# Kernel tuning notes

Measured on AMD Instinct MI355X. Metric: run time of the kernel, lower is better.

## Reference

```python
import jax, jax.numpy as jnp
import numpy as np

# Static config matching init_kwargs
DG = 8          # deformable groups
KH, KW = 3, 3
STRIDE, PAD, DIL = 1, 1, 1


def setup_inputs() -> dict:
    key = jax.random.key(0)
    k1, k2, k3, k4 = jax.random.split(key, 4)
    B, C, H, W = 4, 128, 128, 128
    Cout = 128
    K = KH * KW
    x = jax.random.normal(k1, (B, C, H, W), dtype=jnp.float32)
    offset = jax.random.normal(k2, (B, 2 * DG * K, H, W), dtype=jnp.float32)
    mask = jax.random.uniform(k3, (B, DG * K, H, W), dtype=jnp.float32)
    stdv = 1.0 / np.sqrt(C * KH * KW)
    weight = jax.random.uniform(k4, (Cout, C, KH, KW), dtype=jnp.float32,
                                minval=-stdv, maxval=stdv)
    bias = jnp.zeros((Cout,), dtype=jnp.float32)
    return {"x": x, "offset": offset, "mask": mask, "weight": weight, "bias": bias}


def _deform_conv2d(x, offset, mask, weight, bias):
    B, C, H, W = x.shape
    Cout = weight.shape[0]
    K = KH * KW
    Ho = (H + 2 * PAD - DIL * (KH - 1) - 1) // STRIDE + 1
    Wo = (W + 2 * PAD - DIL * (KW - 1) - 1) // STRIDE + 1
    Cg = C // DG

    # offsets: channel layout [dg, k, (dy, dx)]
    off = offset.reshape(B, DG, K, 2, Ho, Wo)
    dy, dx = off[:, :, :, 0], off[:, :, :, 1]          # [B, DG, K, Ho, Wo]
    m = mask.reshape(B, DG, K, Ho, Wo)

    ky, kx = jnp.meshgrid(jnp.arange(KH), jnp.arange(KW), indexing='ij')
    ky, kx = ky.reshape(K), kx.reshape(K)
    # base sampling grid per kernel tap: [K, Ho] / [K, Wo]
    py = (jnp.arange(Ho) * STRIDE - PAD)[None, :] + (ky * DIL)[:, None]
    px = (jnp.arange(Wo) * STRIDE - PAD)[None, :] + (kx * DIL)[:, None]

    sy = dy + py[None, None, :, :, None].astype(dy.dtype)  # [B, DG, K, Ho, Wo]
    sx = dx + px[None, None, :, None, :].astype(dx.dtype)

    y0f = jnp.floor(sy); x0f = jnp.floor(sx)
    ly = sy - y0f; lx = sx - x0f
    y0 = y0f.astype(jnp.int32); x0 = x0f.astype(jnp.int32)

    x_g = x.reshape(B, DG, Cg, H * W)

    def gather(iy, ix):
        valid = ((iy >= 0) & (iy < H) & (ix >= 0) & (ix < W)).astype(x.dtype)
        idx = jnp.clip(iy, 0, H - 1) * W + jnp.clip(ix, 0, W - 1)
        flat = idx.reshape(B, DG, 1, K * Ho * Wo)
        v = jnp.take_along_axis(x_g, flat, axis=3).reshape(B, DG, Cg, K, Ho, Wo)
        return v * valid[:, :, None]

    w00 = ((1 - ly) * (1 - lx))[:, :, None]
    w01 = ((1 - ly) * lx)[:, :, None]
    w10 = (ly * (1 - lx))[:, :, None]
    w11 = (ly * lx)[:, :, None]

    val = (gather(y0, x0) * w00 + gather(y0, x0 + 1) * w01 +
           gather(y0 + 1, x0) * w10 + gather(y0 + 1, x0 + 1) * w11)
    val = val * m[:, :, None]                         # modulation
    sampled = val.reshape(B, C, K, Ho, Wo)

    w = weight.reshape(Cout, C, K)
    out = jnp.einsum('bckhw,ock->bohw', sampled, w)
    return out + bias[None, :, None, None]


def reference(x, offset, mask, weight, bias):
    return _deform_conv2d(x, offset, mask, weight, bias)
```

## Files before the change

### kernel.cpp

```cpp
#include <hip/hip_runtime.h>
#include <hip/hip_fp16.h>


#define NB    4
#define NC    128
#define NH    128
#define NW    128
#define NCOUT 128
#define NDG   8
#define NCG   16
#define NK    9
#define NCK   1152
#define NHW   16384
#define GK    160
#define ROWP  168

typedef __attribute__((ext_vector_type(4))) float f32x4;
typedef _Float16 half8 __attribute__((ext_vector_type(8)));

union C16 { uint4 u[2]; __half2 h[8]; };

__device__ __forceinline__ unsigned pk2h(float a, float b) {
  return (unsigned)__half_as_ushort(__float2half_rn(a)) |
         ((unsigned)__half_as_ushort(__float2half_rn(b)) << 16);
}

__global__ __launch_bounds__(256)
void prep(const float* __restrict__ x, const float* __restrict__ w,
          ushort* __restrict__ xt, ushort* __restrict__ wf) {
  __shared__ __align__(16) unsigned LDSU[1024 * 9];
  const int tid = threadIdx.x;

  if (blockIdx.x < 128) {
    const int o = blockIdx.x;
    float* WL = (float*)LDSU;
    const float4* src = (const float4*)(w + o * NCK);
    for (int i = tid; i < NCK / 4; i += 256) ((float4*)WL)[i] = src[i];
    __syncthreads();
    unsigned* dstw = (unsigned*)wf;
    for (int t = tid; t < 640; t += 256) {
      const int g = t / 80, r = t - g * 80;
      unsigned v = 0;
      if (r < 72) {
        const int k = r >> 3;
        const int c = g * NCG + (r & 7) * 2;
        v = pk2h(WL[c * NK + k], WL[(c + 1) * NK + k]);
      }
      const int ks = r >> 4;
      const int kq = (r >> 2) & 3;
      const int ep = r & 3;
      dstw[((((g * 5 + ks) * 4 + kq) * 128) + o) * 4 + ep] = v;
    }
  } else {
    const int blk  = blockIdx.x - 128;
    const int slab = blk >> 4;
    const int hw0  = (blk & 15) * 1024;
    const float* xb = x + (size_t)slab * NCG * NHW + hw0;
#pragma unroll
    for (int cp = 0; cp < 8; ++cp) {
#pragma unroll
      for (int i = 0; i < 4; ++i) {
        const int hw = tid + 256 * i;
        LDSU[hw * 9 + cp] =
            pk2h(xb[(2 * cp) * NHW + hw], xb[(2 * cp + 1) * NHW + hw]);
      }
    }
    __syncthreads();
    uint4* dst = (uint4*)(xt + ((size_t)slab * NHW + hw0) * NCG);
#pragma unroll
    for (int j = 0; j < 8; ++j) {
      const int lin = tid + 256 * j;
      const int hw = lin >> 1, q = lin & 1;
      uint4 v;
      v.x = LDSU[hw * 9 + q * 4 + 0];
      v.y = LDSU[hw * 9 + q * 4 + 1];
      v.z = LDSU[hw * 9 + q * 4 + 2];
      v.w = LDSU[hw * 9 + q * 4 + 3];
      dst[lin] = v;
    }
  }
}

__device__ __forceinline__ void sample_one(
    int p, int k, int g, int b, int ho, float dy, float dx, float mm,
    const ushort* __restrict__ xt, ushort* __restrict__ S) {
  const int ky = k / 3, kx = k - ky * 3;

  const float sy = dy + (float)(ho - 1 + ky);
  const float sx = dx + (float)(p - 1 + kx);
  const float y0f = floorf(sy), x0f = floorf(sx);
  const float ly = sy - y0f, lx = sx - x0f;
  const int y0 = (int)y0f, x0 = (int)x0f;
  const int y1 = y0 + 1,  x1 = x0 + 1;
  const float hy = 1.f - ly, hx = 1.f - lx;

  float w00 = hy * hx * mm, w01 = hy * lx * mm;
  float w10 = ly * hx * mm, w11 = ly * lx * mm;
  if (y0 < 0 || y0 >= NH) { w00 = 0.f; w01 = 0.f; }
  if (y1 < 0 || y1 >= NH) { w10 = 0.f; w11 = 0.f; }
  if (x0 < 0 || x0 >= NW) { w00 = 0.f; w10 = 0.f; }
  if (x1 < 0 || x1 >= NW) { w01 = 0.f; w11 = 0.f; }

  const int yc0 = min(max(y0, 0), NH - 1);
  const int yc1 = min(max(y1, 0), NH - 1);
  const int xc0 = min(max(x0, 0), NW - 1);
  const int xc1 = min(max(x1, 0), NW - 1);

  const ushort* xg = xt + (size_t)(b * NDG + g) * NHW * NCG;
  const uint4* q00 = (const uint4*)(xg + (yc0 * NW + xc0) * NCG);
  const uint4* q01 = (const uint4*)(xg + (yc0 * NW + xc1) * NCG);
  const uint4* q10 = (const uint4*)(xg + (yc1 * NW + xc0) * NCG);
  const uint4* q11 = (const uint4*)(xg + (yc1 * NW + xc1) * NCG);

  C16 v00, v01, v10, v11, r;
  v00.u[0] = q00[0]; v00.u[1] = q00[1];
  v01.u[0] = q01[0]; v01.u[1] = q01[1];
  v10.u[0] = q10[0]; v10.u[1] = q10[1];
  v11.u[0] = q11[0]; v11.u[1] = q11[1];

  const __half2 W00 = __float2half2_rn(w00);
  const __half2 W01 = __float2half2_rn(w01);
  const __half2 W10 = __float2half2_rn(w10);
  const __half2 W11 = __float2half2_rn(w11);
#pragma unroll
  for (int i = 0; i < 8; ++i) {
    __half2 a = __hmul2(v00.h[i], W00);
    a = __hfma2(v01.h[i], W01, a);
    a = __hfma2(v10.h[i], W10, a);
    a = __hfma2(v11.h[i], W11, a);
    r.h[i] = a;
  }
  ushort* dp = &S[p * ROWP + k * 16];
  *(uint4*)dp = r.u[0];
  *((uint4*)dp + 1) = r.u[1];
}

__global__ __launch_bounds__(512, 4)
void dcn_main(const float* __restrict__ off,
              const float* __restrict__ msk,
              const ushort* __restrict__ xt,
              const ushort* __restrict__ wf,
              const float* __restrict__ bias,
              float* __restrict__ out) {
  __shared__ __align__(16) ushort S[128 * ROWP];

  const int tid  = threadIdx.x;
  const int blk0 = blockIdx.x;
  const int blk  = (blk0 & 7) * 64 + (blk0 >> 3);
  const int b    = blk >> 7;
  const int ho   = blk & 127;

  const int lane = tid & 63;
  const int wv   = tid >> 6;
  const int l15  = lane & 15;
  const int kq   = lane >> 4;
  const int mh   = (wv & 1) * 4;
  const int nb   = wv >> 1;
  const int cbase = nb * 32 + l15;

  const float* offB = off + (size_t)b * 144 * NHW + ho * NW;
  const float* mskB = msk + (size_t)b * 72  * NHW + ho * NW;

  for (int i = tid; i < 128 * 8; i += 512) {
    ((unsigned*)S)[(i >> 3) * (ROWP / 2) + 72 + (i & 7)] = 0;
  }

  f32x4 acc[4][2];
#pragma unroll
  for (int m = 0; m < 4; ++m) {
    acc[m][0] = {0.f, 0.f, 0.f, 0.f};
    acc[m][1] = {0.f, 0.f, 0.f, 0.f};
  }

  const int p0 = tid & 127;
  const int k0 = tid >> 7;
  const int k1 = k0 + 4;

  float dy0, dx0, mm0, dy1, dx1, mm1, dy2 = 0.f, dx2 = 0.f, mm2 = 0.f;
  {
    dy0 = offB[(k0 * 2) * NHW + p0];
    dx0 = offB[(k0 * 2 + 1) * NHW + p0];
    mm0 = mskB[k0 * NHW + p0];
    dy1 = offB[(k1 * 2) * NHW + p0];
    dx1 = offB[(k1 * 2 + 1) * NHW + p0];
    mm1 = mskB[k1 * NHW + p0];
    if (tid < 128) {
      dy2 = offB[16 * NHW + p0];
      dx2 = offB[17 * NHW + p0];
      mm2 = mskB[8 * NHW + p0];
    }
  }

  for (int g = 0; g < 8; ++g) {
    if (g) __syncthreads();

    half8 bf0[5], bf1[5];
    {
      const ushort* wb = wf + ((size_t)(g * 20 + kq) * 128 + cbase) * 8;
#pragma unroll
      for (int ks = 0; ks < 5; ++ks) {
        bf0[ks] = *(const half8*)(wb + ks * 4096);
        bf1[ks] = *(const half8*)(wb + ks * 4096 + 128);
      }
    }

    sample_one(p0, k0, g, b, ho, dy0, dx0, mm0, xt, S);
    sample_one(p0, k1, g, b, ho, dy1, dx1, mm1, xt, S);
    if (tid < 128) sample_one(p0, 8, g, b, ho, dy2, dx2, mm2, xt, S);

    if (g < 7) {
      const int gka = (g + 1) * 9 + k0, gkb = (g + 1) * 9 + k1;
      dy0 = offB[(gka * 2) * NHW + p0];
      dx0 = offB[(gka * 2 + 1) * NHW + p0];
      mm0 = mskB[gka * NHW + p0];
      dy1 = offB[(gkb * 2) * NHW + p0];
      dx1 = offB[(gkb * 2 + 1) * NHW + p0];
      mm1 = mskB[gkb * NHW + p0];
      if (tid < 128) {
        const int gkc = (g + 1) * 9 + 8;
        dy2 = offB[(gkc * 2) * NHW + p0];
        dx2 = offB[(gkc * 2 + 1) * NHW + p0];
        mm2 = mskB[gkc * NHW + p0];
      }
    }
    __syncthreads();

    const ushort* sa = &S[l15 * ROWP + kq * 8];
#pragma unroll
    for (int ks = 0; ks < 5; ++ks) {
#pragma unroll
      for (int m = 0; m < 4; ++m) {
        const half8 a = *(const half8*)(sa + (mh + m) * 16 * ROWP + ks * 32);
        acc[m][0] = __builtin_amdgcn_mfma_f32_16x16x32_f16(a, bf0[ks], acc[m][0], 0, 0, 0);
        acc[m][1] = __builtin_amdgcn_mfma_f32_16x16x32_f16(a, bf1[ks], acc[m][1], 0, 0, 0);
      }
    }
  }

#pragma unroll
  for (int j = 0; j < 2; ++j) {
    const int c0 = nb * 32 + j * 16 + l15;
    const float bs = bias[c0];
    float* op = out + (size_t)(b * NCOUT + c0) * NHW + ho * NW + kq * 4;
#pragma unroll
    for (int m = 0; m < 4; ++m) {
      float4 r = {acc[m][j][0] + bs, acc[m][j][1] + bs,
                  acc[m][j][2] + bs, acc[m][j][3] + bs};
      *(float4*)(op + (mh + m) * 16) = r;
    }
  }
}

extern "C" void kernel_launch(void* const* d_in, const int* in_sizes, int n_in,
                              void* d_out, int out_size, void* d_ws, size_t ws_size,
                              hipStream_t stream) {
  const float* x    = (const float*)d_in[0];
  const float* off  = (const float*)d_in[1];
  const float* msk  = (const float*)d_in[2];
  const float* wgt  = (const float*)d_in[3];
  const float* bias = (const float*)d_in[4];
  float* out = (float*)d_out;

  ushort* xt = (ushort*)d_ws;
  ushort* wf = xt + (size_t)NB * NDG * NHW * NCG;

  hipLaunchKernelGGL(prep, dim3(640), dim3(256), 0, stream, x, wgt, xt, wf);
  hipLaunchKernelGGL(dcn_main, dim3(512), dim3(512), 0, stream,
                     off, msk, xt, wf, bias, out);
}
```

Baseline: 221.4 us.

## Switch GEMM stage to 32x32x16 MFMA with repacked weight fragments

Replaces the 16x16x32 MFMA tiling (4x2 tiles per wave, weights preloaded to registers) with 32x32x16 MFMA, two accumulators per wave. Weight fragments are repacked in prep into a layout matched to the new instruction and loaded per k-step inside the loop instead of being held in registers. The intent is fewer MFMA issues and LDS reads per FLOP and lower register pressure. In exchange, the weight global loads now sit on the critical path after the barrier, and the K dimension is padded to 160.

```diff
diff --git a/kernel.cpp b/kernel.cpp
--- a/kernel.cpp
+++ b/kernel.cpp
@@ -15,7 +15,7 @@
 #define GK    160
 #define ROWP  168
 
-typedef __attribute__((ext_vector_type(4))) float f32x4;
+typedef __attribute__((ext_vector_type(16))) float f32x16;
 typedef _Float16 half8 __attribute__((ext_vector_type(8)));
 
 union C16 { uint4 u[2]; __half2 h[8]; };
@@ -39,17 +39,18 @@
     __syncthreads();
     unsigned* dstw = (unsigned*)wf;
     for (int t = tid; t < 640; t += 256) {
-      const int g = t / 80, r = t - g * 80;
+      const int frag  = t >> 2;
+      const int pairI = t & 3;
+      const int khalf = frag & 1;
+      const int fk    = frag >> 1;
+      const int g     = fk / 10;
+      const int ks    = fk - g * 10;
       unsigned v = 0;
-      if (r < 72) {
-        const int k = r >> 3;
-        const int c = g * NCG + (r & 7) * 2;
-        v = pk2h(WL[c * NK + k], WL[(c + 1) * NK + k]);
+      if (ks < 9) {
+        const int c = g * NCG + khalf * 8 + pairI * 2;
+        v = pk2h(WL[c * NK + ks], WL[(c + 1) * NK + ks]);
       }
-      const int ks = r >> 4;
-      const int kq = (r >> 2) & 3;
-      const int ep = r & 3;
-      dstw[((((g * 5 + ks) * 4 + kq) * 128) + o) * 4 + ep] = v;
+      dstw[frag * 512 + o * 4 + pairI] = v;
     }
   } else {
     const int blk  = blockIdx.x - 128;
@@ -150,27 +151,23 @@
   const int b    = blk >> 7;
   const int ho   = blk & 127;
 
-  const int lane = tid & 63;
-  const int wv   = tid >> 6;
-  const int l15  = lane & 15;
-  const int kq   = lane >> 4;
-  const int mh   = (wv & 1) * 4;
-  const int nb   = wv >> 1;
-  const int cbase = nb * 32 + l15;
+  const int lane  = tid & 63;
+  const int wv    = tid >> 6;
+  const int l31   = lane & 31;
+  const int hi    = lane >> 5;
+  const int nbase = (wv & 3) * 32;
+  const int mpair = wv >> 2;
 
   const float* offB = off + (size_t)b * 144 * NHW + ho * NW;
   const float* mskB = msk + (size_t)b * 72  * NHW + ho * NW;
 
-  for (int i = tid; i < 128 * 8; i += 512) {
+  for (int i = tid; i < 1024; i += 512) {
     ((unsigned*)S)[(i >> 3) * (ROWP / 2) + 72 + (i & 7)] = 0;
   }
 
-  f32x4 acc[4][2];
-#pragma unroll
-  for (int m = 0; m < 4; ++m) {
-    acc[m][0] = {0.f, 0.f, 0.f, 0.f};
-    acc[m][1] = {0.f, 0.f, 0.f, 0.f};
-  }
+  f32x16 acc0, acc1;
+#pragma unroll
+  for (int i = 0; i < 16; ++i) { acc0[i] = 0.f; acc1[i] = 0.f; }
 
   const int p0 = tid & 127;
   const int k0 = tid >> 7;
@@ -193,16 +190,6 @@
 
   for (int g = 0; g < 8; ++g) {
     if (g) __syncthreads();
-
-    half8 bf0[5], bf1[5];
-    {
-      const ushort* wb = wf + ((size_t)(g * 20 + kq) * 128 + cbase) * 8;
-#pragma unroll
-      for (int ks = 0; ks < 5; ++ks) {
-        bf0[ks] = *(const half8*)(wb + ks * 4096);
-        bf1[ks] = *(const half8*)(wb + ks * 4096 + 128);
-      }
-    }
 
     sample_one(p0, k0, g, b, ho, dy0, dx0, mm0, xt, S);
     sample_one(p0, k1, g, b, ho, dy1, dx1, mm1, xt, S);
@@ -225,28 +212,32 @@
     }
     __syncthreads();
 
-    const ushort* sa = &S[l15 * ROWP + kq * 8];
-#pragma unroll
-    for (int ks = 0; ks < 5; ++ks) {
-#pragma unroll
-      for (int m = 0; m < 4; ++m) {
-        const half8 a = *(const half8*)(sa + (mh + m) * 16 * ROWP + ks * 32);
-        acc[m][0] = __builtin_amdgcn_mfma_f32_16x16x32_f16(a, bf0[ks], acc[m][0], 0, 0, 0);
-        acc[m][1] = __builtin_amdgcn_mfma_f32_16x16x32_f16(a, bf1[ks], acc[m][1], 0, 0, 0);
-      }
-    }
-  }
-
+    const ushort* wb  = wf + ((size_t)(g * 10) * 2 + hi) * 1024
+                           + (nbase + l31) * 8;
+    const ushort* sa0 = &S[(mpair * 64 + l31) * ROWP + hi * 8];
+    const ushort* sa1 = sa0 + 32 * ROWP;
+#pragma unroll
+    for (int ks = 0; ks < 10; ++ks) {
+      const half8 bfrag = *(const half8*)(wb + ks * 2048);
+      const half8 a0 = *(const half8*)(sa0 + ks * 16);
+      const half8 a1 = *(const half8*)(sa1 + ks * 16);
+      acc0 = __builtin_amdgcn_mfma_f32_32x32x16_f16(a0, bfrag, acc0, 0, 0, 0);
+      acc1 = __builtin_amdgcn_mfma_f32_32x32x16_f16(a1, bfrag, acc1, 0, 0, 0);
+    }
+  }
+
+  const int cout = nbase + l31;
+  const float bs = bias[cout];
+  float* opb = out + (size_t)(b * NCOUT + cout) * NHW + ho * NW;
 #pragma unroll
   for (int j = 0; j < 2; ++j) {
-    const int c0 = nb * 32 + j * 16 + l15;
-    const float bs = bias[c0];
-    float* op = out + (size_t)(b * NCOUT + c0) * NHW + ho * NW + kq * 4;
-#pragma unroll
-    for (int m = 0; m < 4; ++m) {
-      float4 r = {acc[m][j][0] + bs, acc[m][j][1] + bs,
-                  acc[m][j][2] + bs, acc[m][j][3] + bs};
-      *(float4*)(op + (mh + m) * 16) = r;
+    const f32x16 a = j ? acc1 : acc0;
+    float* op = opb + (mpair * 2 + j) * 32 + hi * 4;
+#pragma unroll
+    for (int r4 = 0; r4 < 4; ++r4) {
+      float4 r = {a[r4 * 4 + 0] + bs, a[r4 * 4 + 1] + bs,
+                  a[r4 * 4 + 2] + bs, a[r4 * 4 + 3] + bs};
+      *(float4*)(op + r4 * 8) = r;
     }
   }
 }
```

After: 186.5 us. -15.8%, faster.
